# Kernel optimization log

Measured on AMD Instinct MI355X. Metric: run time of the kernel, lower is better.

Reference implementation:

```python
import jax, jax.numpy as jnp
import numpy as np
from jax import lax

B, L, D_MODEL = 2, 4096, 1024
D_INNER = 2 * D_MODEL          # expand=2
D_STATE = D_INNER              # required: complex einsum contracts d_inner vs d_state
DT_RANK = 64                   # ceil(1024/16)
D_CONV = 4


def setup_inputs() -> dict:
    key = jax.random.key(0)
    ks = jax.random.split(key, 16)
    s = lambda *sh: 1.0 / np.sqrt(sh[-1])
    return {
        "hidden_states": jax.random.normal(ks[0], (B, L, D_MODEL), jnp.float32),
        "delta": jax.random.normal(ks[1], (B, L, DT_RANK), jnp.float32),
        # in_proj: Linear(d_model -> 2*d_inner), no bias
        "in_proj_w": jax.random.normal(ks[2], (2 * D_INNER, D_MODEL), jnp.float32) * s(D_MODEL),
        # depthwise causal conv1d: (out=d_inner, in/groups=1, k)
        "conv_w": jax.random.normal(ks[3], (D_INNER, 1, D_CONV), jnp.float32) * s(D_CONV),
        "conv_b": jax.random.normal(ks[4], (D_INNER,), jnp.float32) * 0.01,
        # ComplexStateSpace: only A_real affects the real output (x is real)
        "A_real": jax.random.normal(ks[5], (D_STATE, D_STATE), jnp.float32) * 0.1 / np.sqrt(D_STATE),
        # MIMO linears (torch Linear weight layout [out, in])
        "B_w": jax.random.normal(ks[6], (D_STATE, D_INNER), jnp.float32) * 0.1 * s(D_INNER),
        "C_w": jax.random.normal(ks[7], (D_INNER, D_STATE), jnp.float32) * 0.1 * s(D_STATE),
        "D_w": jax.random.normal(ks[8], (D_INNER, D_INNER), jnp.float32) * 0.1 * s(D_INNER),
        # SelectiveScan params
        "dt_proj_w": jax.random.normal(ks[9], (D_INNER, DT_RANK), jnp.float32) * 0.01,
        "dt_proj_b": jax.random.normal(ks[10], (D_INNER,), jnp.float32) * 0.01,
        "A_log": jax.random.uniform(ks[11], (D_INNER,), jnp.float32, -4.0, -1.0),
        "D_ss": jnp.ones((D_INNER,), jnp.float32),
        # out_proj: Linear(d_inner -> d_model), no bias
        "out_proj_w": jax.random.normal(ks[12], (D_MODEL, D_INNER), jnp.float32) * s(D_INNER),
    }


def reference(hidden_states, delta, in_proj_w, conv_w, conv_b, A_real,
              B_w, C_w, D_w, dt_proj_w, dt_proj_b, A_log, D_ss, out_proj_w):
    d_inner = A_log.shape[0]
    # in_proj + split
    xz = jnp.einsum('bld,ed->ble', hidden_states, in_proj_w)
    x, z = xz[..., :d_inner], xz[..., d_inner:]
    # depthwise causal conv1d (left-pad k-1 == torch pad both + truncate to L)
    xc = jnp.swapaxes(x, 1, 2)                      # [b, d, l]
    xc = lax.conv_general_dilated(xc, conv_w, window_strides=(1,),
                                  padding=[(D_CONV - 1, 0)],
                                  feature_group_count=d_inner)
    x = jnp.swapaxes(xc, 1, 2) + conv_b             # [b, l, d]
    x = jax.nn.silu(x)
    # ComplexStateSpace: real part of (x @ (A_real + iA_imag)) == x @ A_real
    x = x + jnp.einsum('bls,st->blt', x, A_real)
    # MIMO SSM: state_t = cumsum(B x)_t ; y_t = C state_t + D x_t  (vectorized)
    Bx = jnp.einsum('bld,sd->bls', x, B_w)          # [b, l, d_state]
    states = jnp.cumsum(Bx, axis=1)
    x_mimo = jnp.einsum('bls,es->ble', states, C_w) + jnp.einsum('bld,ed->ble', x, D_w)
    x = x + x_mimo
    # SelectiveScan: state = state * exp(dlt * A) + u, A = -exp(A_log)
    dlt = jax.nn.softplus(jnp.einsum('blr,dr->bld', delta, dt_proj_w) + dt_proj_b)
    decay = jnp.exp(dlt * (-jnp.exp(A_log)))        # [b, l, d], in (0, 1)

    def step(state, inp):
        dec, u = inp
        state = state * dec + u
        return state, state

    init = jnp.zeros_like(x[:, 0])
    _, scan_states = lax.scan(step, init,
                              (jnp.swapaxes(decay, 0, 1), jnp.swapaxes(x, 0, 1)))
    x = jnp.swapaxes(scan_states, 0, 1) + x * D_ss
    # gate + out projection
    out = x * jax.nn.silu(z)
    return jnp.einsum('ble,de->bld', out, out_proj_w)
```

## Files before the change

### kernel.cpp

```cpp
#include <hip/hip_runtime.h>
#include <cstdint>
#include <cstddef>


typedef unsigned short u16;
typedef __bf16 bf16x8 __attribute__((ext_vector_type(8)));
typedef float  f32x4  __attribute__((ext_vector_type(4)));

#define BDIM 256
#define M_ROWS 8192
#define LSEQ   4096
#define DI     2048
#define NCH    64
#define CLEN   64

__device__ __forceinline__ float bf2f(u16 h) {
    return __uint_as_float(((unsigned int)h) << 16);
}
__device__ __forceinline__ u16 f2bf(float f) {
    unsigned int u = __float_as_uint(f);
    u = u + 0x7fffu + ((u >> 16) & 1u);
    return (u16)(u >> 16);
}
__device__ __forceinline__ float siluf(float v) { return v / (1.0f + expf(-v)); }

__device__ __forceinline__ void load16_to_lds(const u16* g, u16* l) {
    __builtin_amdgcn_global_load_lds((const __attribute__((address_space(1))) void*)g,
                                     (__attribute__((address_space(3))) void*)l,
                                     16, 0, 0);
}

__global__ void k_cvt_all(const float* __restrict__ hs, const float* __restrict__ inproj,
                          const float* __restrict__ Bw, const float* __restrict__ Cw,
                          const float* __restrict__ outw, const float* __restrict__ delta,
                          const float* __restrict__ dtw, const float* __restrict__ Areal,
                          const float* __restrict__ Dw,
                          u16* __restrict__ XH, u16* __restrict__ W1, u16* __restrict__ WBb,
                          u16* __restrict__ WC, u16* __restrict__ WO, u16* __restrict__ DLT,
                          u16* __restrict__ WDT, u16* __restrict__ Pb, u16* __restrict__ Db) {
    long i = (long)(blockIdx.x * BDIM + threadIdx.x) * 4;
    const float* src; u16* dst; long off; bool diag = false;
    if      (i <  8388608L) { src = hs;     dst = XH;  off = 0L; }
    else if (i < 12582912L) { src = inproj; dst = W1;  off = 8388608L; }
    else if (i < 16777216L) { src = Bw;     dst = WBb; off = 12582912L; }
    else if (i < 20971520L) { src = Cw;     dst = WC;  off = 16777216L; }
    else if (i < 23068672L) { src = outw;   dst = WO;  off = 20971520L; }
    else if (i < 23592960L) { src = delta;  dst = DLT; off = 23068672L; }
    else if (i < 23724032L) { src = dtw;    dst = WDT; off = 23592960L; }
    else if (i < 27918336L) { src = Areal;  dst = Pb;  off = 23724032L; diag = true; }
    else                    { src = Dw;     dst = Db;  off = 27918336L; diag = true; }
    long j = i - off;
    float4 v = *reinterpret_cast<const float4*>(src + j);
    if (diag) {
        int r = (int)(j >> 11), c = (int)(j & 2047);
        if (r >= c && r < c + 4) (&v.x)[r - c] += 1.0f;
    }
    ushort2 a = {f2bf(v.x), f2bf(v.y)};
    ushort2 b = {f2bf(v.z), f2bf(v.w)};
    *reinterpret_cast<ushort2*>(dst + j)     = a;
    *reinterpret_cast<ushort2*>(dst + j + 2) = b;
}

__device__ __forceinline__ void gemm_core(
    u16* As, u16* Bs,
    const u16* __restrict__ A1, const u16* __restrict__ W1, int K1,
    const u16* __restrict__ A2, const u16* __restrict__ W2, int K2,
    int N, float* __restrict__ outf, u16* __restrict__ outb, u16* __restrict__ outb2,
    const float* __restrict__ bias1, const float* __restrict__ bias2,
    int m0, int n0, int mode) {
    const int tid  = threadIdx.x;
    const int wave = tid >> 6;
    const int lane = tid & 63;
    const int wm = (wave >> 1) * 64;
    const int wn = (wave & 1) * 64;
    const int lr = lane & 15;
    const int lq = lane >> 4;
    const int stg_row = lane >> 3;
    const int stg_col = (((lane & 7) ^ (lane >> 3)) << 3);

    f32x4 acc[4][4] = {};

    const int nt1 = K1 >> 6;
    const int nt2 = K2 >> 6;
    const int ntot = nt1 + nt2;

    for (int kt = 0; kt < ntot; ++kt) {
        const u16* Ap; const u16* Wp; int ld, k0;
        if (kt < nt1) { Ap = A1; Wp = W1; ld = K1; k0 = kt << 6; }
        else          { Ap = A2; Wp = W2; ld = K2; k0 = (kt - nt1) << 6; }
        #pragma unroll
        for (int i = 0; i < 4; ++i) {
            int chunk = wave * 4 + i;
            int r = chunk * 8 + stg_row;
            load16_to_lds(Ap + (size_t)(m0 + r) * ld + (k0 + stg_col), As + chunk * 512);
            load16_to_lds(Wp + (size_t)(n0 + r) * ld + (k0 + stg_col), Bs + chunk * 512);
        }
        __syncthreads();
        #pragma unroll
        for (int kk = 0; kk < 64; kk += 32) {
            bf16x8 af[4], bfr[4];
            #pragma unroll
            for (int i = 0; i < 4; ++i) {
                int R = wm + i * 16 + lr;
                af[i] = *reinterpret_cast<const bf16x8*>(
                    &As[R * 64 + ((kk + lq * 8) ^ ((R & 7) << 3))]);
            }
            #pragma unroll
            for (int i = 0; i < 4; ++i) {
                int R = wn + i * 16 + lr;
                bfr[i] = *reinterpret_cast<const bf16x8*>(
                    &Bs[R * 64 + ((kk + lq * 8) ^ ((R & 7) << 3))]);
            }
            #pragma unroll
            for (int mi = 0; mi < 4; ++mi)
                #pragma unroll
                for (int ni = 0; ni < 4; ++ni)
                    acc[mi][ni] = __builtin_amdgcn_mfma_f32_16x16x32_bf16(
                        af[mi], bfr[ni], acc[mi][ni], 0, 0, 0);
        }
        __syncthreads();
    }

    #pragma unroll
    for (int mi = 0; mi < 4; ++mi) {
        #pragma unroll
        for (int ni = 0; ni < 4; ++ni) {
            #pragma unroll
            for (int j = 0; j < 4; ++j) {
                int row = m0 + wm + mi * 16 + lq * 4 + j;
                int col = n0 + wn + ni * 16 + lr;
                float v = acc[mi][ni][j];
                if (mode == 6) {
                    if (col < 2048) outb [(size_t)row * 2048 + col]        = f2bf(v);
                    else            outb2[(size_t)row * 2048 + col - 2048] = f2bf(v);
                } else if (mode == 5) {
                    float dlt = v + bias1[col];
                    dlt = (dlt > 15.f) ? dlt : log1pf(expf(dlt));
                    outb[(size_t)row * N + col] = f2bf(-expf(bias2[col]) * dlt);
                } else if (mode == 2) {
                    outf[(size_t)row * N + col] = v;
                } else {
                    outb[(size_t)row * N + col] = f2bf(v);
                }
            }
        }
    }
}

__device__ __forceinline__ void tile_coords(int q, int T, int gn, int& m0, int& n0) {
    int nloc = T >> 3;
    int nid  = (q & 7) * nloc + (q >> 3);
    m0 = (nid / gn) * 128;
    n0 = (nid % gn) * 128;
}

__global__ __launch_bounds__(256, 4)
void k_batch1(const u16* __restrict__ XH, const u16* __restrict__ W1,
              const u16* __restrict__ WBb, const u16* __restrict__ Pb,
              const u16* __restrict__ Db,
              u16* __restrict__ WBp, u16* __restrict__ WXp,
              u16* __restrict__ XB, u16* __restrict__ ZB) {
    __shared__ u16 As[128 * 64];
    __shared__ u16 Bs[128 * 64];
    int bid = blockIdx.x;
    int m0, n0;
    if (bid < 256) {
        tile_coords(bid, 256, 16, m0, n0);
        gemm_core(As, Bs, WBb, Pb, DI, nullptr, nullptr, 0, DI,
                  nullptr, WBp, nullptr, nullptr, nullptr, m0, n0, 0);
    } else if (bid < 512) {
        tile_coords(bid - 256, 256, 16, m0, n0);
        gemm_core(As, Bs, Db, Pb, DI, nullptr, nullptr, 0, DI,
                  nullptr, WXp, nullptr, nullptr, nullptr, m0, n0, 0);
    } else {
        tile_coords(bid - 512, 2048, 32, m0, n0);
        gemm_core(As, Bs, XH, W1, 1024, nullptr, nullptr, 0, 4096,
                  nullptr, XB, ZB, nullptr, nullptr, m0, n0, 6);
    }
}

__global__ __launch_bounds__(256, 4)
void k_batch2(const u16* __restrict__ XC, const u16* __restrict__ WBp,
              const u16* __restrict__ DLT, const u16* __restrict__ WDT,
              const float* __restrict__ dtb, const float* __restrict__ Alog,
              u16* __restrict__ BX, u16* __restrict__ LD) {
    __shared__ u16 As[128 * 64];
    __shared__ u16 Bs[128 * 64];
    int bid = blockIdx.x;
    int m0, n0;
    if (bid < 1024) {
        tile_coords(bid, 1024, 16, m0, n0);
        gemm_core(As, Bs, XC, WBp, DI, nullptr, nullptr, 0, DI,
                  nullptr, BX, nullptr, nullptr, nullptr, m0, n0, 0);
    } else {
        tile_coords(bid - 1024, 1024, 16, m0, n0);
        gemm_core(As, Bs, DLT, WDT, 64, nullptr, nullptr, 0, DI,
                  nullptr, LD, nullptr, dtb, Alog, m0, n0, 5);
    }
}

template <int MODE>
__global__ __launch_bounds__(256, 4)
void k_gemm(const u16* __restrict__ A1, const u16* __restrict__ W1, int K1,
            const u16* __restrict__ A2, const u16* __restrict__ W2, int K2,
            int N, float* __restrict__ outf, u16* __restrict__ outb) {
    __shared__ u16 As[128 * 64];
    __shared__ u16 Bs[128 * 64];
    int bid = blockIdx.x + gridDim.x * blockIdx.y;
    int m0, n0;
    tile_coords(bid, gridDim.x * gridDim.y, gridDim.x, m0, n0);
    gemm_core(As, Bs, A1, W1, K1, A2, W2, K2, N,
              outf, outb, nullptr, nullptr, nullptr, m0, n0, MODE);
}

__global__ void k_conv(const u16* __restrict__ x, const float* __restrict__ w,
                       const float* __restrict__ b, u16* __restrict__ out) {
    int idx = blockIdx.x * BDIM + threadIdx.x;
    int d  = idx & (DI - 1);
    int bl = idx >> 11;
    int l  = bl & (LSEQ - 1);
    float4 wv = *reinterpret_cast<const float4*>(w + d * 4);
    float wj[4] = {wv.x, wv.y, wv.z, wv.w};
    float acc = b[d];
    #pragma unroll
    for (int j = 0; j < 4; ++j) {
        int ll = l - 3 + j;
        if (ll >= 0) acc += wj[j] * bf2f(x[(size_t)(bl - 3 + j) * DI + d]);
    }
    out[idx] = f2bf(siluf(acc));
}

__global__ void k_cumsum_p1(const u16* __restrict__ Bx, float* __restrict__ aux) {
    int t = blockIdx.x * BDIM + threadIdx.x;
    int s = t & (DI - 1);
    int c = (t >> 11) & (NCH - 1);
    int b = t >> 17;
    const u16* p = Bx + ((size_t)(b * LSEQ + c * CLEN) * DI) + s;
    float sum = 0.f;
    for (int i = 0; i < CLEN; ++i) sum += bf2f(p[(size_t)i * DI]);
    aux[t] = sum;
}
__global__ void k_cumsum_p23(const u16* __restrict__ Bx, const float* __restrict__ aux,
                             u16* __restrict__ st) {
    int t = blockIdx.x * BDIM + threadIdx.x;
    int s = t & (DI - 1);
    int c = (t >> 11) & (NCH - 1);
    int b = t >> 17;
    float run = 0.f;
    for (int j = 0; j < c; ++j) run += aux[(b * NCH + j) * DI + s];
    size_t base = ((size_t)(b * LSEQ + c * CLEN) * DI) + s;
    for (int i = 0; i < CLEN; ++i) {
        run += bf2f(Bx[base + (size_t)i * DI]);
        st[base + (size_t)i * DI] = f2bf(run);
    }
}

__global__ void k_scan_p1(const u16* __restrict__ ld_, const u16* __restrict__ u,
                          float* __restrict__ auxA, float* __restrict__ auxS) {
    int t = blockIdx.x * BDIM + threadIdx.x;
    int d = t & (DI - 1);
    int c = (t >> 11) & (NCH - 1);
    int b = t >> 17;
    size_t base = ((size_t)(b * LSEQ + c * CLEN) * DI) + d;
    float ap = 1.f, s = 0.f;
    for (int i = 0; i < CLEN; ++i) {
        size_t ix = base + (size_t)i * DI;
        float a = expf(bf2f(ld_[ix]));
        s = fmaf(a, s, bf2f(u[ix]));
        ap *= a;
    }
    auxA[t] = ap; auxS[t] = s;
}
__global__ void k_scan_p23(const u16* __restrict__ ld_, const u16* __restrict__ u,
                           const float* __restrict__ auxA, const float* __restrict__ auxS,
                           const u16* __restrict__ z, const float* __restrict__ Dss,
                           u16* __restrict__ outb) {
    int t = blockIdx.x * BDIM + threadIdx.x;
    int d = t & (DI - 1);
    int c = (t >> 11) & (NCH - 1);
    int b = t >> 17;
    float s = 0.f;
    for (int j = 0; j < c; ++j) {
        int i = (b * NCH + j) * DI + d;
        s = fmaf(auxA[i], s, auxS[i]);
    }
    size_t base = ((size_t)(b * LSEQ + c * CLEN) * DI) + d;
    float dss = Dss[d];
    for (int i = 0; i < CLEN; ++i) {
        size_t ix = base + (size_t)i * DI;
        float a = expf(bf2f(ld_[ix]));
        float uu = bf2f(u[ix]);
        s = fmaf(a, s, uu);
        float x4 = s + uu * dss;
        float zz = bf2f(z[ix]);
        outb[ix] = f2bf(x4 * siluf(zz));
    }
}

extern "C" void kernel_launch(void* const* d_in, const int* in_sizes, int n_in,
                              void* d_out, int out_size, void* d_ws, size_t ws_size,
                              hipStream_t stream) {
    const float* hs     = (const float*)d_in[0];
    const float* delta  = (const float*)d_in[1];
    const float* inproj = (const float*)d_in[2];
    const float* convw  = (const float*)d_in[3];
    const float* convb  = (const float*)d_in[4];
    const float* Areal  = (const float*)d_in[5];
    const float* Bw     = (const float*)d_in[6];
    const float* Cw     = (const float*)d_in[7];
    const float* Dw     = (const float*)d_in[8];
    const float* dtw    = (const float*)d_in[9];
    const float* dtb    = (const float*)d_in[10];
    const float* Alog   = (const float*)d_in[11];
    const float* Dss    = (const float*)d_in[12];
    const float* outw   = (const float*)d_in[13];
    float* out = (float*)d_out;

    const size_t SZ_ACT = (size_t)M_ROWS * DI * 2;
    char* p = (char*)d_ws;
    u16* ZB  = (u16*)p; p += SZ_ACT;
    u16* XB  = (u16*)p;
    u16* X3  = XB;      p += SZ_ACT;
    u16* XC  = (u16*)p;
    u16* OUT = XC;      p += SZ_ACT;
    u16* BX  = (u16*)p; p += SZ_ACT;
    u16* ST  = (u16*)p; p += SZ_ACT;
    u16* XH  = (u16*)p;
    u16* LD  = XH;
                        p += (size_t)M_ROWS * 1024 * 2;
    u16* W1  = (u16*)p; p += (size_t)4096 * 1024 * 2;
    u16* WBb = (u16*)p; p += (size_t)DI * DI * 2;
    u16* WC  = (u16*)p; p += (size_t)DI * DI * 2;
    u16* Pb  = (u16*)p; p += (size_t)DI * DI * 2;
    u16* Db  = (u16*)p; p += (size_t)DI * DI * 2;
    u16* WBp = (u16*)p; p += (size_t)DI * DI * 2;
    u16* WXp = (u16*)p; p += (size_t)DI * DI * 2;
    u16* WO  = (u16*)p; p += (size_t)1024 * DI * 2;
    u16* WDT = (u16*)p; p += (size_t)DI * 64 * 2;
    u16* DLT = (u16*)p; p += (size_t)M_ROWS * 64 * 2;
    float* aux1 = (float*)p; p += (size_t)2 * NCH * DI * 4;
    float* auxA = (float*)p; p += (size_t)2 * NCH * DI * 4;
    float* auxS = (float*)p; p += (size_t)2 * NCH * DI * 4;

    k_cvt_all<<<31360, BDIM, 0, stream>>>(hs, inproj, Bw, Cw, outw, delta, dtw,
                                          Areal, Dw,
                                          XH, W1, WBb, WC, WO, DLT, WDT, Pb, Db);
    k_batch1<<<2560, BDIM, 0, stream>>>(XH, W1, WBb, Pb, Db, WBp, WXp, XB, ZB);
    k_conv<<<(M_ROWS * DI) / BDIM, BDIM, 0, stream>>>(XB, convw, convb, XC);
    k_batch2<<<2048, BDIM, 0, stream>>>(XC, WBp, DLT, WDT, dtb, Alog, BX, LD);
    k_cumsum_p1<<<(2 * NCH * DI) / BDIM, BDIM, 0, stream>>>(BX, aux1);
    k_cumsum_p23<<<(2 * NCH * DI) / BDIM, BDIM, 0, stream>>>(BX, aux1, ST);
    k_gemm<0><<<dim3(16, 64), BDIM, 0, stream>>>(ST, WC, DI, XC, WXp, DI,
                                                 DI, nullptr, X3);
    k_scan_p1<<<(2 * NCH * DI) / BDIM, BDIM, 0, stream>>>(LD, X3, auxA, auxS);
    k_scan_p23<<<(2 * NCH * DI) / BDIM, BDIM, 0, stream>>>(LD, X3, auxA, auxS,
                                                           ZB, Dss, OUT);
    k_gemm<2><<<dim3(8, 64), BDIM, 0, stream>>>(OUT, WO, DI, nullptr, nullptr, 0,
                                                1024, out, nullptr);
}
```

Measured before the change: 712.8 us.

## Fold C projection into B weights so cumsum runs after C instead of before

Uses linearity of the cumsum to precompute a combined (P·B)·C weight matrix (computed in a transposed-output GEMM mode fused into the conv launch), so the MIMO state path becomes cumsum(x·W_CB). This removes the separate cumsum output buffer and drops the second A-operand stream from the big C-projection GEMM, which now only computes x·W_X. The cumsum kernel adds its running sum into the X3 buffer in place. A small 2048x2048 weight GEMM is added per call, and rounding happens at a different point in bf16.

```diff
diff --git a/kernel.cpp b/kernel.cpp
--- a/kernel.cpp
+++ b/kernel.cpp
@@ -121,6 +121,22 @@
         __syncthreads();
     }
 
+    if (mode == 8) {
+        #pragma unroll
+        for (int mi = 0; mi < 4; ++mi) {
+            #pragma unroll
+            for (int ni = 0; ni < 4; ++ni) {
+                int row = m0 + wm + mi * 16 + lq * 4;
+                int col = n0 + wn + ni * 16 + lr;
+                ushort4 v;
+                v.x = f2bf(acc[mi][ni][0]); v.y = f2bf(acc[mi][ni][1]);
+                v.z = f2bf(acc[mi][ni][2]); v.w = f2bf(acc[mi][ni][3]);
+                *reinterpret_cast<ushort4*>(outb + (size_t)col * 2048 + row) = v;
+            }
+        }
+        return;
+    }
+
     #pragma unroll
     for (int mi = 0; mi < 4; ++mi) {
         #pragma unroll
@@ -158,7 +174,7 @@
 void k_batch1(const u16* __restrict__ XH, const u16* __restrict__ W1,
               const u16* __restrict__ WBb, const u16* __restrict__ Pb,
               const u16* __restrict__ Db,
-              u16* __restrict__ WBp, u16* __restrict__ WXp,
+              u16* __restrict__ PBt, u16* __restrict__ WXp,
               u16* __restrict__ XB, u16* __restrict__ ZB) {
     __shared__ u16 As[128 * 64];
     __shared__ u16 Bs[128 * 64];
@@ -166,8 +182,8 @@
     int m0, n0;
     if (bid < 256) {
         tile_coords(bid, 256, 16, m0, n0);
-        gemm_core(As, Bs, WBb, Pb, DI, nullptr, nullptr, 0, DI,
-                  nullptr, WBp, nullptr, nullptr, nullptr, m0, n0, 0);
+        gemm_core(As, Bs, Pb, WBb, DI, nullptr, nullptr, 0, DI,
+                  nullptr, PBt, nullptr, nullptr, nullptr, m0, n0, 0);
     } else if (bid < 512) {
         tile_coords(bid - 256, 256, 16, m0, n0);
         gemm_core(As, Bs, Db, Pb, DI, nullptr, nullptr, 0, DI,
@@ -180,18 +196,47 @@
 }
 
 __global__ __launch_bounds__(256, 4)
-void k_batch2(const u16* __restrict__ XC, const u16* __restrict__ WBp,
+void k_conv_pre3(const u16* __restrict__ x, const float* __restrict__ w,
+                 const float* __restrict__ b, u16* __restrict__ out,
+                 const u16* __restrict__ PBt, const u16* __restrict__ WC,
+                 u16* __restrict__ WCBp) {
+    __shared__ u16 As[128 * 64];
+    __shared__ u16 Bs[128 * 64];
+    if (blockIdx.x < 256) {
+        int m0, n0;
+        tile_coords(blockIdx.x, 256, 16, m0, n0);
+        gemm_core(As, Bs, PBt, WC, DI, nullptr, nullptr, 0, DI,
+                  nullptr, WCBp, nullptr, nullptr, nullptr, m0, n0, 8);
+        return;
+    }
+    int idx = (blockIdx.x - 256) * BDIM + threadIdx.x;
+    int d  = idx & (DI - 1);
+    int bl = idx >> 11;
+    int l  = bl & (LSEQ - 1);
+    float4 wv = *reinterpret_cast<const float4*>(w + d * 4);
+    float wj[4] = {wv.x, wv.y, wv.z, wv.w};
+    float acc = b[d];
+    #pragma unroll
+    for (int j = 0; j < 4; ++j) {
+        int ll = l - 3 + j;
+        if (ll >= 0) acc += wj[j] * bf2f(x[(size_t)(bl - 3 + j) * DI + d]);
+    }
+    out[idx] = f2bf(siluf(acc));
+}
+
+__global__ __launch_bounds__(256, 4)
+void k_batch2(const u16* __restrict__ XC, const u16* __restrict__ WCBp,
               const u16* __restrict__ DLT, const u16* __restrict__ WDT,
               const float* __restrict__ dtb, const float* __restrict__ Alog,
-              u16* __restrict__ BX, u16* __restrict__ LD) {
+              u16* __restrict__ BXC, u16* __restrict__ LD) {
     __shared__ u16 As[128 * 64];
     __shared__ u16 Bs[128 * 64];
     int bid = blockIdx.x;
     int m0, n0;
     if (bid < 1024) {
         tile_coords(bid, 1024, 16, m0, n0);
-        gemm_core(As, Bs, XC, WBp, DI, nullptr, nullptr, 0, DI,
-                  nullptr, BX, nullptr, nullptr, nullptr, m0, n0, 0);
+        gemm_core(As, Bs, XC, WCBp, DI, nullptr, nullptr, 0, DI,
+                  nullptr, BXC, nullptr, nullptr, nullptr, m0, n0, 0);
     } else {
         tile_coords(bid - 1024, 1024, 16, m0, n0);
         gemm_core(As, Bs, DLT, WDT, 64, nullptr, nullptr, 0, DI,
@@ -213,23 +258,6 @@
               outf, outb, nullptr, nullptr, nullptr, m0, n0, MODE);
 }
 
-__global__ void k_conv(const u16* __restrict__ x, const float* __restrict__ w,
-                       const float* __restrict__ b, u16* __restrict__ out) {
-    int idx = blockIdx.x * BDIM + threadIdx.x;
-    int d  = idx & (DI - 1);
-    int bl = idx >> 11;
-    int l  = bl & (LSEQ - 1);
-    float4 wv = *reinterpret_cast<const float4*>(w + d * 4);
-    float wj[4] = {wv.x, wv.y, wv.z, wv.w};
-    float acc = b[d];
-    #pragma unroll
-    for (int j = 0; j < 4; ++j) {
-        int ll = l - 3 + j;
-        if (ll >= 0) acc += wj[j] * bf2f(x[(size_t)(bl - 3 + j) * DI + d]);
-    }
-    out[idx] = f2bf(siluf(acc));
-}
-
 __global__ void k_cumsum_p1(const u16* __restrict__ Bx, float* __restrict__ aux) {
     int t = blockIdx.x * BDIM + threadIdx.x;
     int s = t & (DI - 1);
@@ -241,7 +269,7 @@
     aux[t] = sum;
 }
 __global__ void k_cumsum_p23(const u16* __restrict__ Bx, const float* __restrict__ aux,
-                             u16* __restrict__ st) {
+                             u16* x3) {
     int t = blockIdx.x * BDIM + threadIdx.x;
     int s = t & (DI - 1);
     int c = (t >> 11) & (NCH - 1);
@@ -250,8 +278,9 @@
     for (int j = 0; j < c; ++j) run += aux[(b * NCH + j) * DI + s];
     size_t base = ((size_t)(b * LSEQ + c * CLEN) * DI) + s;
     for (int i = 0; i < CLEN; ++i) {
-        run += bf2f(Bx[base + (size_t)i * DI]);
-        st[base + (size_t)i * DI] = f2bf(run);
+        size_t ix = base + (size_t)i * DI;
+        run += bf2f(Bx[ix]);
+        x3[ix] = f2bf(run + bf2f(x3[ix]));
     }
 }
 
@@ -323,8 +352,8 @@
     u16* X3  = XB;      p += SZ_ACT;
     u16* XC  = (u16*)p;
     u16* OUT = XC;      p += SZ_ACT;
-    u16* BX  = (u16*)p; p += SZ_ACT;
-    u16* ST  = (u16*)p; p += SZ_ACT;
+    u16* BXC = (u16*)p; p += SZ_ACT;
+    u16* WCBp= (u16*)p; p += SZ_ACT;
     u16* XH  = (u16*)p;
     u16* LD  = XH;
                         p += (size_t)M_ROWS * 1024 * 2;
@@ -333,7 +362,7 @@
     u16* WC  = (u16*)p; p += (size_t)DI * DI * 2;
     u16* Pb  = (u16*)p; p += (size_t)DI * DI * 2;
     u16* Db  = (u16*)p; p += (size_t)DI * DI * 2;
-    u16* WBp = (u16*)p; p += (size_t)DI * DI * 2;
+    u16* PBt = (u16*)p; p += (size_t)DI * DI * 2;
     u16* WXp = (u16*)p; p += (size_t)DI * DI * 2;
     u16* WO  = (u16*)p; p += (size_t)1024 * DI * 2;
     u16* WDT = (u16*)p; p += (size_t)DI * 64 * 2;
@@ -345,13 +374,14 @@
     k_cvt_all<<<31360, BDIM, 0, stream>>>(hs, inproj, Bw, Cw, outw, delta, dtw,
                                           Areal, Dw,
                                           XH, W1, WBb, WC, WO, DLT, WDT, Pb, Db);
-    k_batch1<<<2560, BDIM, 0, stream>>>(XH, W1, WBb, Pb, Db, WBp, WXp, XB, ZB);
-    k_conv<<<(M_ROWS * DI) / BDIM, BDIM, 0, stream>>>(XB, convw, convb, XC);
-    k_batch2<<<2048, BDIM, 0, stream>>>(XC, WBp, DLT, WDT, dtb, Alog, BX, LD);
-    k_cumsum_p1<<<(2 * NCH * DI) / BDIM, BDIM, 0, stream>>>(BX, aux1);
-    k_cumsum_p23<<<(2 * NCH * DI) / BDIM, BDIM, 0, stream>>>(BX, aux1, ST);
-    k_gemm<0><<<dim3(16, 64), BDIM, 0, stream>>>(ST, WC, DI, XC, WXp, DI,
+    k_batch1<<<2560, BDIM, 0, stream>>>(XH, W1, WBb, Pb, Db, PBt, WXp, XB, ZB);
+    k_conv_pre3<<<256 + (M_ROWS * DI) / BDIM, BDIM, 0, stream>>>(
+        XB, convw, convb, XC, PBt, WC, WCBp);
+    k_batch2<<<2048, BDIM, 0, stream>>>(XC, WCBp, DLT, WDT, dtb, Alog, BXC, LD);
+    k_cumsum_p1<<<(2 * NCH * DI) / BDIM, BDIM, 0, stream>>>(BXC, aux1);
+    k_gemm<0><<<dim3(16, 64), BDIM, 0, stream>>>(XC, WXp, DI, nullptr, nullptr, 0,
                                                  DI, nullptr, X3);
+    k_cumsum_p23<<<(2 * NCH * DI) / BDIM, BDIM, 0, stream>>>(BXC, aux1, X3);
     k_scan_p1<<<(2 * NCH * DI) / BDIM, BDIM, 0, stream>>>(LD, X3, auxA, auxS);
     k_scan_p23<<<(2 * NCH * DI) / BDIM, BDIM, 0, stream>>>(LD, X3, auxA, auxS,
                                                            ZB, Dss, OUT);
```

After: 727.8 us. 1.02x slower.
